# Optimization experiments

Measured on AMD Instinct MI355X. Metric: run time of the kernel, lower is better.

The kernel has to match this reference:

```python
import jax, jax.numpy as jnp
import numpy as np

SIGMA_XY = 15.0
SIGMA_RGB = 0.125
B, C, H, W = 1, 1, 96, 96


def setup_inputs() -> dict:
    key = jax.random.key(0)
    k1, k2 = jax.random.split(key)
    inp = jax.random.uniform(k1, (B, C, H, W), dtype=jnp.float32)   # segmentation probs in [0,1]
    img = jax.random.uniform(k2, (B, 3, H, W), dtype=jnp.float32)   # RGB in [0,1]
    return {"input": inp, "image": img}


def _crf_loss_single(s, img, pos):
    # s: [C, N] probs, img: [3, N] colors, pos: [N, 2] scaled xy coords
    feat = jnp.concatenate([pos, img.T / SIGMA_RGB], axis=1)        # [N, 5] joint bilateral features
    sq = jnp.sum(feat * feat, axis=1)                                # [N]
    d2 = sq[:, None] + sq[None, :] - 2.0 * (feat @ feat.T)           # [N, N] squared feature distance
    Wm = jnp.exp(-0.5 * jnp.maximum(d2, 0.0))                        # [N, N] Gaussian bilateral affinity
    # dense CRF relaxed Potts loss: sum_c s_c^T W (1 - s_c)
    return jnp.sum((Wm @ (1.0 - s.T)) * s.T)


def reference(input, image):
    b, c, h, w = input.shape
    n = h * w
    yy, xx = jnp.meshgrid(jnp.arange(h, dtype=input.dtype),
                          jnp.arange(w, dtype=input.dtype), indexing="ij")
    pos = jnp.stack([xx, yy], axis=-1).reshape(n, 2) / SIGMA_XY      # [N, 2]
    s = input.reshape(b, c, n)
    img = image.reshape(b, 3, n)
    losses = jax.vmap(lambda sv, iv: _crf_loss_single(sv, iv, pos))(s, img)
    return jnp.sum(losses) / n                                        # per-pixel normalized scalar loss
```

## Files before the change

### kernel.cpp

```cpp
#include <hip/hip_runtime.h>

#define NPTS   9216
#define WIDTH  96
#define CHUNK  1024
#define NCHUNK 9
#define NPAIR  45
#define JSUB   64
#define NJSUB  16
#define IPT    4

#define KSCALE 1.2011224087864498f

typedef _Float16 half2v __attribute__((ext_vector_type(2)));
union H2F { half2v h; float f; };

__global__ __launch_bounds__(256)
void crf_feat_kernel(const float* __restrict__ s,
                     const float* __restrict__ img,
                     float4* __restrict__ arrF,
                     float* __restrict__ arrS,
                     float* __restrict__ out) {
    int p = blockIdx.x * 256 + threadIdx.x;
    if (p == 0) out[0] = 0.0f;
    if (p >= NPTS) return;
    int y = p / WIDTH;
    int x = p - y * WIDTH;
    float sv = s[p];
    float xs = (float)x * (KSCALE / 15.0f);
    float ys = (float)y * (KSCALE / 15.0f);
    float rs = img[p]          * (8.0f * KSCALE);
    float gs = img[NPTS + p]   * (8.0f * KSCALE);
    float bs = img[2*NPTS + p] * (8.0f * KSCALE);
    _Float16 xh = (_Float16)xs, yh = (_Float16)ys;
    _Float16 rh = (_Float16)rs, gh = (_Float16)gs, bh = (_Float16)bs;
    float xr = (float)xh, yr = (float)yh, rr = (float)rh, gr = (float)gh, br = (float)bh;
    float hs = -0.5f * (xr*xr + yr*yr + rr*rr + gr*gr + br*br);

    H2F xy; xy.h = half2v{xh, yh};
    H2F rg; rg.h = half2v{rh, gh};
    H2F b0; b0.h = half2v{bh, (_Float16)sv};

    float4 r;
    r.x = xy.f; r.y = rg.f; r.z = b0.f; r.w = hs;
    arrF[p] = r;
    arrS[p] = sv;
}

__global__ __launch_bounds__(256)
void crf_pair_kernel(const float4* __restrict__ arrF,
                     const float* __restrict__ arrS,
                     float* __restrict__ out) {
    __shared__ float4 shF[JSUB];
    __shared__ float wavesum[4];

    const int tid = threadIdx.x;

    int p = blockIdx.x, a = 0;
    while (p >= NCHUNK - a) { p -= NCHUNK - a; ++a; }
    const int b = a + p;
    const int ibase = a * CHUNK;
    const int jbase = b * CHUNK + blockIdx.y * JSUB;

    if (tid < JSUB) shF[tid] = arrF[jbase + tid];

    half2v xyi[IPT], rgi[IPT], b0i[IPT];
    float  hsi[IPT], svi[IPT];
    #pragma unroll
    for (int k = 0; k < IPT; ++k) {
        int i = ibase + k * 256 + tid;
        float4 r = arrF[i];
        H2F u; u.f = r.x; xyi[k] = u.h;
        H2F v; v.f = r.y; rgi[k] = v.h;
        H2F w; w.f = r.z; w.h.y = (_Float16)0.0f; b0i[k] = w.h;
        hsi[k] = r.w;
        svi[k] = arrS[i];
    }

    __syncthreads();

    float A[IPT] = {0.f, 0.f, 0.f, 0.f};
    float B[IPT] = {0.f, 0.f, 0.f, 0.f};

    #pragma unroll 4
    for (int j = 0; j < JSUB; ++j) {
        float4 fj = shF[j];
        H2F u; u.f = fj.x;
        H2F v; v.f = fj.y;
        H2F w; w.f = fj.z;
        const half2v xyj = u.h, rgj = v.h, bsj = w.h;
        const float sjf = (float)w.h.y;
        #pragma unroll
        for (int k = 0; k < IPT; ++k) {
            float e = hsi[k] + fj.w;
            e = __builtin_amdgcn_fdot2(xyi[k], xyj, e, false);
            e = __builtin_amdgcn_fdot2(rgi[k], rgj, e, false);
            e = __builtin_amdgcn_fdot2(b0i[k], bsj, e, false);
            float wv = __builtin_amdgcn_exp2f(e);
            A[k] += wv;
            B[k] = fmaf(wv, sjf, B[k]);
        }
    }

    float t = 0.0f;
    #pragma unroll
    for (int k = 0; k < IPT; ++k)
        t += svi[k] * A[k] + fmaf(-2.0f * svi[k], B[k], B[k]);

    const float wt = (a == b) ? 0.5f : 1.0f;
    t *= wt * (1.0f / (float)NPTS);

    #pragma unroll
    for (int off = 32; off > 0; off >>= 1)
        t += __shfl_down(t, off, 64);
    if ((tid & 63) == 0) wavesum[tid >> 6] = t;
    __syncthreads();
    if (tid == 0)
        atomicAdd(out, wavesum[0] + wavesum[1] + wavesum[2] + wavesum[3]);
}

extern "C" void kernel_launch(void* const* d_in, const int* in_sizes, int n_in,
                              void* d_out, int out_size, void* d_ws, size_t ws_size,
                              hipStream_t stream) {
    const float* s   = (const float*)d_in[0];
    const float* img = (const float*)d_in[1];
    float* out = (float*)d_out;

    float4* arrF = (float4*)d_ws;
    float*  arrS = (float*)(arrF + NPTS);

    crf_feat_kernel<<<NPTS/256, 256, 0, stream>>>(s, img, arrF, arrS, out);
    dim3 grid(NPAIR, NJSUB);
    crf_pair_kernel<<<grid, 256, 0, stream>>>(arrF, arrS, out);
}
```

Measured before the change: 71.16 us.

## Fuse feature computation into pair kernel and double j-tile size

Removes the separate feature-precompute kernel and its workspace round trip: each pair block now computes the i-point and j-point features directly from the raw inputs, and the output is zeroed with a memset. The j sub-tile per block is doubled, which halves the grid and gives each block twice the pairwise work to amortise the recomputed features. The cost is redundant feature math and strided loads of the raw inputs in every block, plus fewer blocks to spread across the GPU.

```diff
diff --git a/kernel.cpp b/kernel.cpp
--- a/kernel.cpp
+++ b/kernel.cpp
@@ -5,8 +5,8 @@
 #define CHUNK  1024
 #define NCHUNK 9
 #define NPAIR  45
-#define JSUB   64
-#define NJSUB  16
+#define JSUB   128
+#define NJSUB  8
 #define IPT    4
 
 #define KSCALE 1.2011224087864498f
@@ -14,42 +14,32 @@
 typedef _Float16 half2v __attribute__((ext_vector_type(2)));
 union H2F { half2v h; float f; };
 
-__global__ __launch_bounds__(256)
-void crf_feat_kernel(const float* __restrict__ s,
-                     const float* __restrict__ img,
-                     float4* __restrict__ arrF,
-                     float* __restrict__ arrS,
-                     float* __restrict__ out) {
-    int p = blockIdx.x * 256 + threadIdx.x;
-    if (p == 0) out[0] = 0.0f;
-    if (p >= NPTS) return;
-    int y = p / WIDTH;
-    int x = p - y * WIDTH;
-    float sv = s[p];
-    float xs = (float)x * (KSCALE / 15.0f);
-    float ys = (float)y * (KSCALE / 15.0f);
-    float rs = img[p]          * (8.0f * KSCALE);
-    float gs = img[NPTS + p]   * (8.0f * KSCALE);
-    float bs = img[2*NPTS + p] * (8.0f * KSCALE);
+__device__ __forceinline__ void make_feat(int q, const float* __restrict__ s,
+                                          const float* __restrict__ img,
+                                          bool carry_s,
+                                          half2v& xy, half2v& rg, half2v& bs2,
+                                          float& hs, float& sv) {
+    int yy = q / WIDTH;
+    int xx = q - yy * WIDTH;
+    sv = s[q];
+    float xs = (float)xx * (KSCALE / 15.0f);
+    float ys = (float)yy * (KSCALE / 15.0f);
+    float rs = img[q]          * (8.0f * KSCALE);
+    float gs = img[NPTS + q]   * (8.0f * KSCALE);
+    float bs = img[2*NPTS + q] * (8.0f * KSCALE);
     _Float16 xh = (_Float16)xs, yh = (_Float16)ys;
     _Float16 rh = (_Float16)rs, gh = (_Float16)gs, bh = (_Float16)bs;
     float xr = (float)xh, yr = (float)yh, rr = (float)rh, gr = (float)gh, br = (float)bh;
-    float hs = -0.5f * (xr*xr + yr*yr + rr*rr + gr*gr + br*br);
-
-    H2F xy; xy.h = half2v{xh, yh};
-    H2F rg; rg.h = half2v{rh, gh};
-    H2F b0; b0.h = half2v{bh, (_Float16)sv};
-
-    float4 r;
-    r.x = xy.f; r.y = rg.f; r.z = b0.f; r.w = hs;
-    arrF[p] = r;
-    arrS[p] = sv;
+    hs = -0.5f * (xr*xr + yr*yr + rr*rr + gr*gr + br*br);
+    xy  = half2v{xh, yh};
+    rg  = half2v{rh, gh};
+    bs2 = half2v{bh, carry_s ? (_Float16)sv : (_Float16)0.0f};
 }
 
 __global__ __launch_bounds__(256)
-void crf_pair_kernel(const float4* __restrict__ arrF,
-                     const float* __restrict__ arrS,
-                     float* __restrict__ out) {
+void crf_fused_kernel(const float* __restrict__ s,
+                      const float* __restrict__ img,
+                      float* __restrict__ out) {
     __shared__ float4 shF[JSUB];
     __shared__ float wavesum[4];
 
@@ -61,20 +51,21 @@
     const int ibase = a * CHUNK;
     const int jbase = b * CHUNK + blockIdx.y * JSUB;
 
-    if (tid < JSUB) shF[tid] = arrF[jbase + tid];
+    if (tid < JSUB) {
+        half2v xy, rg, bs2; float hs, sv;
+        make_feat(jbase + tid, s, img, true, xy, rg, bs2, hs, sv);
+        H2F u; u.h = xy;
+        H2F v; v.h = rg;
+        H2F w; w.h = bs2;
+        shF[tid] = float4{u.f, v.f, w.f, hs};
+    }
 
     half2v xyi[IPT], rgi[IPT], b0i[IPT];
     float  hsi[IPT], svi[IPT];
     #pragma unroll
-    for (int k = 0; k < IPT; ++k) {
-        int i = ibase + k * 256 + tid;
-        float4 r = arrF[i];
-        H2F u; u.f = r.x; xyi[k] = u.h;
-        H2F v; v.f = r.y; rgi[k] = v.h;
-        H2F w; w.f = r.z; w.h.y = (_Float16)0.0f; b0i[k] = w.h;
-        hsi[k] = r.w;
-        svi[k] = arrS[i];
-    }
+    for (int k = 0; k < IPT; ++k)
+        make_feat(ibase + k * 256 + tid, s, img, false,
+                  xyi[k], rgi[k], b0i[k], hsi[k], svi[k]);
 
     __syncthreads();
 
@@ -125,10 +116,8 @@
     const float* img = (const float*)d_in[1];
     float* out = (float*)d_out;
 
-    float4* arrF = (float4*)d_ws;
-    float*  arrS = (float*)(arrF + NPTS);
+    hipMemsetAsync(out, 0, sizeof(float), stream);
 
-    crf_feat_kernel<<<NPTS/256, 256, 0, stream>>>(s, img, arrF, arrS, out);
     dim3 grid(NPAIR, NJSUB);
-    crf_pair_kernel<<<grid, 256, 0, stream>>>(arrF, arrS, out);
+    crf_fused_kernel<<<grid, 256, 0, stream>>>(s, img, out);
 }
```

Result: slower. 73.24 us (+2.9%).
